# Kernel optimization log

Hardware: AMD Instinct MI355X
Metric: run time of the kernel (lower is better)

## Reference

```python
import jax, jax.numpy as jnp
import numpy as np

B, S, D = 4, 2048, 512
H, DK, DV = 8, 64, 64

def setup_inputs() -> dict:
    key = jax.random.key(0)
    ks = jax.random.split(key, 11)
    s = 0.02
    return {
        "q_in": jax.random.normal(ks[0], (B, S, D), jnp.float32),
        "k_in": jax.random.normal(ks[1], (B, S, D), jnp.float32),
        "v_in": jax.random.normal(ks[2], (B, S, D), jnp.float32),
        "Wq": jax.random.normal(ks[3], (H, D, DK), jnp.float32) * s,
        "bq": jax.random.normal(ks[4], (H, DK), jnp.float32) * s,
        "Wk": jax.random.normal(ks[5], (H, D, DK), jnp.float32) * s,
        "bk": jax.random.normal(ks[6], (H, DK), jnp.float32) * s,
        "Wv": jax.random.normal(ks[7], (H, D, DV), jnp.float32) * s,
        "bv": jax.random.normal(ks[8], (H, DV), jnp.float32) * s,
        "Wo": jax.random.normal(ks[9], (H * DV, D), jnp.float32) * s,
        "bo": jax.random.normal(ks[10], (D,), jnp.float32) * s,
    }


def reference(q_in, k_in, v_in, Wq, bq, Wk, bk, Wv, bv, Wo, bo):
    # Per-head Q/K/V projections, batched over heads (same math as the
    # original Python loop over SingleAttention heads).
    q = jnp.einsum("bsd,hdk->bhsk", q_in, Wq) + bq[None, :, None, :]   # [B,H,S,DK]
    k = jnp.einsum("bsd,hdk->bhsk", k_in, Wk) + bk[None, :, None, :]   # [B,H,S,DK]
    v = jnp.einsum("bsd,hdv->bhsv", v_in, Wv) + bv[None, :, None, :]   # [B,H,S,DV]
    scale = 1.0 / jnp.sqrt(jnp.float32(DK))
    scores = jnp.einsum("bhqk,bhsk->bhqs", q, k) * scale               # [B,H,S,S]
    attn = jax.nn.softmax(scores, axis=-1)
    out = jnp.einsum("bhqs,bhsv->bhqv", attn, v)                        # [B,H,S,DV]
    # concat heads along feature dim: [B,S,H*DV]
    concat = out.transpose(0, 2, 1, 3).reshape(B, S, H * DV)
    return concat @ Wo + bo                                             # [B,S,D]
```

## Files before the change

kernel.cpp:

```cpp
#include <hip/hip_runtime.h>
#include <hip/hip_bf16.h>

using bf16 = __hip_bfloat16;
typedef short short8  __attribute__((ext_vector_type(8)));
typedef short short4v __attribute__((ext_vector_type(4)));
typedef float float4v __attribute__((ext_vector_type(4)));

#define MFMA_BF16 __builtin_amdgcn_mfma_f32_16x16x32_bf16

#define B_  4
#define S_  2048
#define D_  512
#define H_  8
#define DK_ 64


__device__ __forceinline__ short f2bf(float f) {
  bf16 h = __float2bfloat16(f);
  return *reinterpret_cast<short*>(&h);
}

__global__ __launch_bounds__(256)
void transpose_w(const float* __restrict__ Wq, const float* __restrict__ Wk,
                 const float* __restrict__ Wv, const float* __restrict__ Wo,
                 short* __restrict__ WqT, short* __restrict__ WkT,
                 short* __restrict__ WvT, short* __restrict__ WoT) {
  __shared__ float tile[64 * 65];
  const int mat = blockIdx.y, t = blockIdx.x, tid = threadIdx.x;
  const float* W = (mat == 0) ? Wq : (mat == 1) ? Wk : (mat == 2) ? Wv : Wo;
  short* T       = (mat == 0) ? WqT : (mat == 1) ? WkT : (mat == 2) ? WvT : WoT;

  size_t sbase, ss, dbase;
  if (mat < 3) {
    int hh = t >> 3, d0 = (t & 7) * 64;
    sbase = (size_t)hh * 32768 + (size_t)d0 * 64;
    ss = 64;
    dbase = (size_t)hh * 64 * 512 + d0;
  } else {
    int n0 = (t >> 3) * 64, k0 = (t & 7) * 64;
    sbase = (size_t)k0 * 512 + n0;
    ss = 512;
    dbase = (size_t)n0 * 512 + k0;
  }

  {
    int r = tid >> 2, c0 = (tid & 3) * 16;
#pragma unroll
    for (int j = 0; j < 4; j++)
      *(float4v*)&tile[r * 65 + c0 + j * 4] =
          *(const float4v*)&W[sbase + (size_t)r * ss + c0 + j * 4];
  }
  __syncthreads();
  {
    int c = tid >> 2, r0 = (tid & 3) * 16;
#pragma unroll
    for (int j = 0; j < 2; j++) {
      short8 s;
#pragma unroll
      for (int u = 0; u < 8; u++) s[u] = f2bf(tile[(r0 + j * 8 + u) * 65 + c]);
      *(short8*)&T[dbase + (size_t)c * 512 + r0 + j * 8] = s;
    }
  }
}

__device__ __forceinline__ void gemm_core(const void* __restrict__ A,
                                          const short* __restrict__ Bt,
                                          int m0, int n0, int fp32,
                                          short* As, short* Bs,
                                          float4v acc[4][4]) {
  const int tid  = threadIdx.x;
  const int lane = tid & 63, wave = tid >> 6;
  const int quad = lane >> 4, l16 = lane & 15;
  const int wm = (wave >> 1) * 64, wn = (wave & 1) * 64;

  for (int k0 = 0; k0 < 512; k0 += 64) {
    __syncthreads();
    if (fp32) {
      const float* Af = (const float*)A;
#pragma unroll
      for (int i = 0; i < 4; i++) {
        int cid = tid + 256 * i;
        int row = cid >> 3, kc = (cid & 7) * 8;
        size_t base = (size_t)(m0 + row) * 512 + k0 + kc;
        float4v f0 = *(const float4v*)&Af[base];
        float4v f1 = *(const float4v*)&Af[base + 4];
        short8 s;
#pragma unroll
        for (int j = 0; j < 4; j++) { s[j] = f2bf(f0[j]); s[j + 4] = f2bf(f1[j]); }
        *(short8*)&As[row * 72 + kc] = s;
        *(short8*)&Bs[row * 72 + kc] =
            *(const short8*)&Bt[(size_t)(n0 + row) * 512 + k0 + kc];
      }
    } else {
      const short* Ab = (const short*)A;
#pragma unroll
      for (int i = 0; i < 4; i++) {
        int cid = tid + 256 * i;
        int row = cid >> 3, kc = (cid & 7) * 8;
        *(short8*)&As[row * 72 + kc] =
            *(const short8*)&Ab[(size_t)(m0 + row) * 512 + k0 + kc];
        *(short8*)&Bs[row * 72 + kc] =
            *(const short8*)&Bt[(size_t)(n0 + row) * 512 + k0 + kc];
      }
    }
    __syncthreads();
#pragma unroll
    for (int ks = 0; ks < 64; ks += 32) {
      short8 af[4], bfr[4];
#pragma unroll
      for (int mi = 0; mi < 4; mi++)
        af[mi] = *(short8*)&As[(wm + mi * 16 + l16) * 72 + ks + quad * 8];
#pragma unroll
      for (int ni = 0; ni < 4; ni++)
        bfr[ni] = *(short8*)&Bs[(wn + ni * 16 + l16) * 72 + ks + quad * 8];
#pragma unroll
      for (int mi = 0; mi < 4; mi++)
#pragma unroll
        for (int ni = 0; ni < 4; ni++)
          acc[mi][ni] = MFMA_BF16(af[mi], bfr[ni], acc[mi][ni], 0, 0, 0);
    }
  }
}

__global__ __launch_bounds__(256, 2)
void qkv_gemm(const float* __restrict__ qin, const float* __restrict__ kin,
              const float* __restrict__ vin,
              const short* __restrict__ WqT, const short* __restrict__ WkT,
              const short* __restrict__ WvT,
              const float* __restrict__ bq, const float* __restrict__ bk,
              const float* __restrict__ bv,
              short* __restrict__ Qp, short* __restrict__ Kp,
              short* __restrict__ Vt) {
  __shared__ __align__(16) short As[128 * 72];
  __shared__ __align__(16) short Bs[128 * 72];
  const int m0 = blockIdx.x * 128, n0 = blockIdx.y * 128;
  const int z = blockIdx.z;
  const float* A    = (z == 0) ? qin : (z == 1) ? kin : vin;
  const short* Bt   = (z == 0) ? WqT : (z == 1) ? WkT : WvT;
  const float* bias = (z == 0) ? bq  : (z == 1) ? bk  : bv;
  const float scale = (z == 0) ? 0.125f * 1.44269504088896f : 1.0f;

  float4v acc[4][4];
#pragma unroll
  for (int mi = 0; mi < 4; mi++)
#pragma unroll
    for (int ni = 0; ni < 4; ni++) acc[mi][ni] = (float4v){0.f, 0.f, 0.f, 0.f};

  gemm_core((const void*)A, Bt, m0, n0, 1, As, Bs, acc);

  const int lane = threadIdx.x & 63, wave = threadIdx.x >> 6;
  const int quad = lane >> 4, l16 = lane & 15;
  const int wm = (wave >> 1) * 64, wn = (wave & 1) * 64;

  if (z < 2) {
    short* out = (z == 0) ? Qp : Kp;
#pragma unroll
    for (int mi = 0; mi < 4; mi++) {
      int m = m0 + wm + mi * 16 + quad * 4;
      int b = m >> 11, s = m & 2047;
#pragma unroll
      for (int ni = 0; ni < 4; ni++) {
        int n = n0 + wn + ni * 16 + l16;
        int h = n >> 6, dk = n & 63;
        float bb = bias[n];
        size_t base = (((size_t)b * H_ + h) * S_ + s) * 64 + dk;
#pragma unroll
        for (int r = 0; r < 4; r++)
          out[base + (size_t)r * 64] = f2bf((acc[mi][ni][r] + bb) * scale);
      }
    }
  } else {
#pragma unroll
    for (int mi = 0; mi < 4; mi++) {
      int m = m0 + wm + mi * 16 + quad * 4;
      int b = m >> 11, s = m & 2047;
#pragma unroll
      for (int ni = 0; ni < 4; ni++) {
        int n = n0 + wn + ni * 16 + l16;
        int h = n >> 6, v = n & 63;
        float bb = bias[n];
        short4v pk;
#pragma unroll
        for (int r = 0; r < 4; r++) pk[r] = f2bf(acc[mi][ni][r] + bb);
        *(short4v*)&Vt[(((size_t)b * H_ + h) * 64 + v) * S_ + s] = pk;
      }
    }
  }
}

__global__ __launch_bounds__(256, 4)
void attn_kernel(const short* __restrict__ Qp, const short* __restrict__ Kp,
                 const short* __restrict__ Vt, short* __restrict__ Ao) {
  __shared__ __align__(16) short Ps[64 * 72];
  __shared__ __align__(16) short Ks[64 * 72];
  __shared__ __align__(16) short Vs[64 * 72];

  const int qt = blockIdx.x, bh = blockIdx.y;
  const int b = bh >> 3, h = bh & 7;
  const int tid = threadIdx.x;
  const int lane = tid & 63, wave = tid >> 6;
  const int quad = lane >> 4, l16 = lane & 15;

  const short* Qb = Qp + (size_t)bh * S_ * 64 + (size_t)qt * 64 * 64;
  const short* Kb = Kp + (size_t)bh * S_ * 64;
  const short* Vb = Vt + (size_t)bh * 64 * S_;

#pragma unroll
  for (int i = 0; i < 2; i++) {
    int cid = tid + 256 * i;
    int row = cid >> 3, kc = (cid & 7) * 8;
    *(short8*)&Ps[row * 72 + kc] = *(const short8*)&Qb[(size_t)row * 64 + kc];
  }
  __syncthreads();

  short8 qf[2];
#pragma unroll
  for (int kk = 0; kk < 2; kk++)
    qf[kk] = *(short8*)&Ps[(wave * 16 + l16) * 72 + kk * 32 + quad * 8];

  float4v lrow = (float4v){0.f, 0.f, 0.f, 0.f};
  float4v acco[4];
#pragma unroll
  for (int ni = 0; ni < 4; ni++) acco[ni] = (float4v){0.f, 0.f, 0.f, 0.f};

  short* Pw = Ps + wave * 16 * 72;

  for (int kv0 = 0; kv0 < S_; kv0 += 64) {
    __syncthreads();
#pragma unroll
    for (int i = 0; i < 2; i++) {
      int cid = tid + 256 * i;
      int row = cid >> 3, kc = (cid & 7) * 8;
      *(short8*)&Ks[row * 72 + kc] =
          *(const short8*)&Kb[(size_t)(kv0 + row) * 64 + kc];
      *(short8*)&Vs[row * 72 + kc] =
          *(const short8*)&Vb[(size_t)row * S_ + kv0 + kc];
    }
    __syncthreads();

    float4v sa[4];
#pragma unroll
    for (int ni = 0; ni < 4; ni++) sa[ni] = (float4v){0.f, 0.f, 0.f, 0.f};
#pragma unroll
    for (int kk = 0; kk < 2; kk++) {
      short8 kf[4];
#pragma unroll
      for (int ni = 0; ni < 4; ni++)
        kf[ni] = *(short8*)&Ks[(ni * 16 + l16) * 72 + kk * 32 + quad * 8];
#pragma unroll
      for (int ni = 0; ni < 4; ni++)
        sa[ni] = MFMA_BF16(qf[kk], kf[ni], sa[ni], 0, 0, 0);
    }

#pragma unroll
    for (int ni = 0; ni < 4; ni++)
#pragma unroll
      for (int r = 0; r < 4; r++) {
        float p = exp2f(sa[ni][r]);
        lrow[r] += p;
        Pw[(quad * 4 + r) * 72 + ni * 16 + l16] = f2bf(p);
      }

#pragma unroll
    for (int kks = 0; kks < 2; kks++) {
      short8 pa = *(short8*)&Pw[l16 * 72 + kks * 32 + quad * 8];
      short8 vb2[4];
#pragma unroll
      for (int ni = 0; ni < 4; ni++)
        vb2[ni] = *(short8*)&Vs[(ni * 16 + l16) * 72 + kks * 32 + quad * 8];
#pragma unroll
      for (int ni = 0; ni < 4; ni++)
        acco[ni] = MFMA_BF16(pa, vb2[ni], acco[ni], 0, 0, 0);
    }
  }

#pragma unroll
  for (int off = 1; off < 16; off <<= 1)
#pragma unroll
    for (int r = 0; r < 4; r++) lrow[r] += __shfl_xor(lrow[r], off, 16);

  const size_t obase = ((size_t)b * S_ + qt * 64 + wave * 16) * D_ + h * 64;
#pragma unroll
  for (int r = 0; r < 4; r++) {
    float li = 1.0f / lrow[r];
    int srow = quad * 4 + r;
#pragma unroll
    for (int ni = 0; ni < 4; ni++)
      Ao[obase + (size_t)srow * D_ + ni * 16 + l16] = f2bf(acco[ni][r] * li);
  }
}

__global__ __launch_bounds__(256, 2)
void out_gemm(const short* __restrict__ A, const short* __restrict__ Bt,
              const float* __restrict__ bias, float* __restrict__ out) {
  __shared__ __align__(16) short As[128 * 72];
  __shared__ __align__(16) short Bs[128 * 72];
  const int m0 = blockIdx.x * 128, n0 = blockIdx.y * 128;

  float4v acc[4][4];
#pragma unroll
  for (int mi = 0; mi < 4; mi++)
#pragma unroll
    for (int ni = 0; ni < 4; ni++) acc[mi][ni] = (float4v){0.f, 0.f, 0.f, 0.f};

  gemm_core((const void*)A, Bt, m0, n0, 0, As, Bs, acc);

  const int lane = threadIdx.x & 63, wave = threadIdx.x >> 6;
  const int quad = lane >> 4, l16 = lane & 15;
  const int wm = (wave >> 1) * 64, wn = (wave & 1) * 64;
#pragma unroll
  for (int mi = 0; mi < 4; mi++) {
    int m = m0 + wm + mi * 16 + quad * 4;
#pragma unroll
    for (int ni = 0; ni < 4; ni++) {
      int n = n0 + wn + ni * 16 + l16;
      float bb = bias[n];
#pragma unroll
      for (int r = 0; r < 4; r++)
        out[(size_t)(m + r) * 512 + n] = acc[mi][ni][r] + bb;
    }
  }
}

extern "C" void kernel_launch(void* const* d_in, const int* in_sizes, int n_in,
                              void* d_out, int out_size, void* d_ws, size_t ws_size,
                              hipStream_t stream) {
  const float* qin = (const float*)d_in[0];
  const float* kin = (const float*)d_in[1];
  const float* vin = (const float*)d_in[2];
  const float* Wq  = (const float*)d_in[3];
  const float* bq  = (const float*)d_in[4];
  const float* Wk  = (const float*)d_in[5];
  const float* bk  = (const float*)d_in[6];
  const float* Wv  = (const float*)d_in[7];
  const float* bv  = (const float*)d_in[8];
  const float* Wo  = (const float*)d_in[9];
  const float* bo  = (const float*)d_in[10];
  float* out = (float*)d_out;
  short* ws  = (short*)d_ws;

  const size_t NTOK = (size_t)B_ * S_ * D_;
  short* Qp  = ws;
  short* Kp  = ws + NTOK;
  short* Vt  = ws + 2 * NTOK;
  short* Ao  = ws + 3 * NTOK;
  short* WqT = ws + 4 * NTOK;
  short* WkT = WqT + 512 * 512;
  short* WvT = WkT + 512 * 512;
  short* WoT = WvT + 512 * 512;

  transpose_w<<<dim3(64, 4), 256, 0, stream>>>(Wq, Wk, Wv, Wo,
                                               WqT, WkT, WvT, WoT);
  qkv_gemm<<<dim3(64, 4, 3), 256, 0, stream>>>(qin, kin, vin, WqT, WkT, WvT,
                                               bq, bk, bv, Qp, Kp, Vt);
  attn_kernel<<<dim3(32, 32), 256, 0, stream>>>(Qp, Kp, Vt, Ao);
  out_gemm<<<dim3(64, 4), 256, 0, stream>>>(Ao, WoT, bo, out);
}
```

Baseline: 220.6 us.

## Rewrite attention kernel with 32x32 MFMA, async double-buffered LDS, register-resident P

The attention kernel now uses 32x32x16 MFMAs with 128 query rows per block (32 per wave). K/V tiles are double-buffered through direct global-to-LDS loads into XOR-swizzled shared memory. Q fragments are loaded straight from global into registers, and P is repacked with cvt_pk and permlane32_swap instead of a round trip through LDS. The change also remaps blocks so neighbouring blocks share a head, and adds s_setprio hints. These aim to cut LDS traffic, barriers and load latency, at the cost of higher register pressure and fewer blocks in the grid.

```diff
diff --git a/kernel.cpp b/kernel.cpp
--- a/kernel.cpp
+++ b/kernel.cpp
@@ -5,8 +5,11 @@
 typedef short short8  __attribute__((ext_vector_type(8)));
 typedef short short4v __attribute__((ext_vector_type(4)));
 typedef float float4v __attribute__((ext_vector_type(4)));
-
-#define MFMA_BF16 __builtin_amdgcn_mfma_f32_16x16x32_bf16
+typedef float f32x16  __attribute__((ext_vector_type(16)));
+typedef unsigned int uint4v __attribute__((ext_vector_type(4)));
+
+#define MFMA_BF16   __builtin_amdgcn_mfma_f32_16x16x32_bf16
+#define MFMA32_BF16 __builtin_amdgcn_mfma_f32_32x32x16_bf16
 
 #define B_  4
 #define S_  2048
@@ -18,6 +21,23 @@
 __device__ __forceinline__ short f2bf(float f) {
   bf16 h = __float2bfloat16(f);
   return *reinterpret_cast<short*>(&h);
+}
+
+__device__ __forceinline__ unsigned cvtpk(float lo, float hi) {
+  unsigned r;
+  asm("v_cvt_pk_bf16_f32 %0, %1, %2" : "=v"(r) : "v"(lo), "v"(hi));
+  return r;
+}
+
+__device__ __forceinline__ void plswap(unsigned& a, unsigned& b) {
+  asm("v_permlane32_swap_b32 %0, %1" : "+v"(a), "+v"(b));
+}
+
+__device__ __forceinline__ short8 mk8(unsigned v0, unsigned v1, unsigned v2,
+                                      unsigned v3) {
+  uint4v u;
+  u[0] = v0; u[1] = v1; u[2] = v2; u[3] = v3;
+  return __builtin_bit_cast(short8, u);
 }
 
 __global__ __launch_bounds__(256)
@@ -191,102 +211,129 @@
 __global__ __launch_bounds__(256, 4)
 void attn_kernel(const short* __restrict__ Qp, const short* __restrict__ Kp,
                  const short* __restrict__ Vt, short* __restrict__ Ao) {
-  __shared__ __align__(16) short Ps[64 * 72];
-  __shared__ __align__(16) short Ks[64 * 72];
-  __shared__ __align__(16) short Vs[64 * 72];
-
-  const int qt = blockIdx.x, bh = blockIdx.y;
+  __shared__ __align__(16) short Ksh[2][4096];
+  __shared__ __align__(16) short Vsh[2][4096];
+
+  const int orig = blockIdx.y * gridDim.x + blockIdx.x;
+  const int lb = (orig & 7) * 64 + (orig >> 3);
+  const int qt = lb & 15, bh = lb >> 4;
   const int b = bh >> 3, h = bh & 7;
+
   const int tid = threadIdx.x;
   const int lane = tid & 63, wave = tid >> 6;
-  const int quad = lane >> 4, l16 = lane & 15;
-
-  const short* Qb = Qp + (size_t)bh * S_ * 64 + (size_t)qt * 64 * 64;
+  const int l31 = lane & 31, hi = lane >> 5, s7 = l31 & 7;
+
+  const short* Qb = Qp + (size_t)bh * S_ * 64;
   const short* Kb = Kp + (size_t)bh * S_ * 64;
   const short* Vb = Vt + (size_t)bh * 64 * S_;
 
-#pragma unroll
-  for (int i = 0; i < 2; i++) {
-    int cid = tid + 256 * i;
-    int row = cid >> 3, kc = (cid & 7) * 8;
-    *(short8*)&Ps[row * 72 + kc] = *(const short8*)&Qb[(size_t)row * 64 + kc];
+  short8 qf[4];
+  {
+    const short* qrow = Qb + (size_t)(qt * 128 + wave * 32 + l31) * 64;
+#pragma unroll
+    for (int w = 0; w < 4; w++)
+      qf[w] = *(const short8*)&qrow[w * 16 + hi * 8];
+  }
+
+  const int slot0 = wave * 128 + lane;
+  const int kr0 = slot0 >> 3, kc0 = slot0 & 7;
+  const int kr1 = kr0 + 8;
+  const short* kg0 = Kb + (size_t)kr0 * 64 + ((kc0 ^ (kr0 & 7)) << 3);
+  const short* kg1 = Kb + (size_t)kr1 * 64 + ((kc0 ^ (kr1 & 7)) << 3);
+  const short* vg0 = Vb + (size_t)kr0 * S_ + ((kc0 ^ (kr0 & 7)) << 3);
+  const short* vg1 = Vb + (size_t)kr1 * S_ + ((kc0 ^ (kr1 & 7)) << 3);
+
+#define GLL(g, l) __builtin_amdgcn_global_load_lds(                        \
+      (const __attribute__((address_space(1))) void*)(g),                  \
+      (__attribute__((address_space(3))) void*)(l), 16, 0, 0)
+
+  f32x16 acc0, acc1;
+#pragma unroll
+  for (int r = 0; r < 16; r++) { acc0[r] = 0.f; acc1[r] = 0.f; }
+  float ls0 = 0.f, ls1 = 0.f;
+
+  {
+    short* kd = &Ksh[0][wave * 1024];
+    short* vd = &Vsh[0][wave * 1024];
+    GLL(kg0, kd); GLL(kg1, kd + 512);
+    GLL(vg0, vd); GLL(vg1, vd + 512);
   }
   __syncthreads();
 
-  short8 qf[2];
-#pragma unroll
-  for (int kk = 0; kk < 2; kk++)
-    qf[kk] = *(short8*)&Ps[(wave * 16 + l16) * 72 + kk * 32 + quad * 8];
-
-  float4v lrow = (float4v){0.f, 0.f, 0.f, 0.f};
-  float4v acco[4];
-#pragma unroll
-  for (int ni = 0; ni < 4; ni++) acco[ni] = (float4v){0.f, 0.f, 0.f, 0.f};
-
-  short* Pw = Ps + wave * 16 * 72;
-
-  for (int kv0 = 0; kv0 < S_; kv0 += 64) {
+  for (int t = 0; t < 32; t++) {
+    const int cur = t & 1;
+    if (t < 31) {
+      short* kd = &Ksh[cur ^ 1][wave * 1024];
+      short* vd = &Vsh[cur ^ 1][wave * 1024];
+      GLL(kg0 + (size_t)(t + 1) * 4096, kd);
+      GLL(kg1 + (size_t)(t + 1) * 4096, kd + 512);
+      GLL(vg0 + (size_t)(t + 1) * 64, vd);
+      GLL(vg1 + (size_t)(t + 1) * 64, vd + 512);
+    }
+    const short* kb = Ksh[cur];
+    const short* vs = Vsh[cur];
+
+#pragma unroll
+    for (int kt = 0; kt < 2; kt++) {
+      f32x16 sa;
+#pragma unroll
+      for (int r = 0; r < 16; r++) sa[r] = 0.f;
+      __builtin_amdgcn_s_setprio(1);
+#pragma unroll
+      for (int w = 0; w < 4; w++) {
+        short8 kf = *(const short8*)&kb[(kt * 32 + l31) * 64 +
+                                        (((2 * w + hi) ^ s7) << 3)];
+        sa = MFMA32_BF16(kf, qf[w], sa, 0, 0, 0);
+      }
+      __builtin_amdgcn_s_setprio(0);
+
+      float pv[16];
+#pragma unroll
+      for (int r = 0; r < 16; r++) pv[r] = exp2f(sa[r]);
+#pragma unroll
+      for (int r = 0; r < 8; r++) { ls0 += pv[r]; ls1 += pv[r + 8]; }
+
+      unsigned a0 = cvtpk(pv[0], pv[1]),  b0 = cvtpk(pv[4], pv[5]);
+      plswap(a0, b0);
+      unsigned c0 = cvtpk(pv[2], pv[3]),  d0 = cvtpk(pv[6], pv[7]);
+      plswap(c0, d0);
+      short8 pa0 = mk8(a0, c0, b0, d0);
+      unsigned a1 = cvtpk(pv[8], pv[9]),  b1 = cvtpk(pv[12], pv[13]);
+      plswap(a1, b1);
+      unsigned c1 = cvtpk(pv[10], pv[11]), d1 = cvtpk(pv[14], pv[15]);
+      plswap(c1, d1);
+      short8 pa1 = mk8(a1, c1, b1, d1);
+
+      __builtin_amdgcn_s_setprio(1);
+      {
+        const int kw0 = kt * 2, kw1 = kt * 2 + 1;
+        short8 v00 = *(const short8*)&vs[l31 * 64 + (((2 * kw0 + hi) ^ s7) << 3)];
+        short8 v10 = *(const short8*)&vs[(32 + l31) * 64 + (((2 * kw0 + hi) ^ s7) << 3)];
+        acc0 = MFMA32_BF16(pa0, v00, acc0, 0, 0, 0);
+        acc1 = MFMA32_BF16(pa0, v10, acc1, 0, 0, 0);
+        short8 v01 = *(const short8*)&vs[l31 * 64 + (((2 * kw1 + hi) ^ s7) << 3)];
+        short8 v11 = *(const short8*)&vs[(32 + l31) * 64 + (((2 * kw1 + hi) ^ s7) << 3)];
+        acc0 = MFMA32_BF16(pa1, v01, acc0, 0, 0, 0);
+        acc1 = MFMA32_BF16(pa1, v11, acc1, 0, 0, 0);
+      }
+      __builtin_amdgcn_s_setprio(0);
+    }
     __syncthreads();
-#pragma unroll
-    for (int i = 0; i < 2; i++) {
-      int cid = tid + 256 * i;
-      int row = cid >> 3, kc = (cid & 7) * 8;
-      *(short8*)&Ks[row * 72 + kc] =
-          *(const short8*)&Kb[(size_t)(kv0 + row) * 64 + kc];
-      *(short8*)&Vs[row * 72 + kc] =
-          *(const short8*)&Vb[(size_t)row * S_ + kv0 + kc];
-    }
-    __syncthreads();
-
-    float4v sa[4];
-#pragma unroll
-    for (int ni = 0; ni < 4; ni++) sa[ni] = (float4v){0.f, 0.f, 0.f, 0.f};
-#pragma unroll
-    for (int kk = 0; kk < 2; kk++) {
-      short8 kf[4];
-#pragma unroll
-      for (int ni = 0; ni < 4; ni++)
-        kf[ni] = *(short8*)&Ks[(ni * 16 + l16) * 72 + kk * 32 + quad * 8];
-#pragma unroll
-      for (int ni = 0; ni < 4; ni++)
-        sa[ni] = MFMA_BF16(qf[kk], kf[ni], sa[ni], 0, 0, 0);
-    }
-
-#pragma unroll
-    for (int ni = 0; ni < 4; ni++)
-#pragma unroll
-      for (int r = 0; r < 4; r++) {
-        float p = exp2f(sa[ni][r]);
-        lrow[r] += p;
-        Pw[(quad * 4 + r) * 72 + ni * 16 + l16] = f2bf(p);
-      }
-
-#pragma unroll
-    for (int kks = 0; kks < 2; kks++) {
-      short8 pa = *(short8*)&Pw[l16 * 72 + kks * 32 + quad * 8];
-      short8 vb2[4];
-#pragma unroll
-      for (int ni = 0; ni < 4; ni++)
-        vb2[ni] = *(short8*)&Vs[(ni * 16 + l16) * 72 + kks * 32 + quad * 8];
-#pragma unroll
-      for (int ni = 0; ni < 4; ni++)
-        acco[ni] = MFMA_BF16(pa, vb2[ni], acco[ni], 0, 0, 0);
-    }
-  }
-
-#pragma unroll
-  for (int off = 1; off < 16; off <<= 1)
-#pragma unroll
-    for (int r = 0; r < 4; r++) lrow[r] += __shfl_xor(lrow[r], off, 16);
-
-  const size_t obase = ((size_t)b * S_ + qt * 64 + wave * 16) * D_ + h * 64;
-#pragma unroll
-  for (int r = 0; r < 4; r++) {
-    float li = 1.0f / lrow[r];
-    int srow = quad * 4 + r;
-#pragma unroll
-    for (int ni = 0; ni < 4; ni++)
-      Ao[obase + (size_t)srow * D_ + ni * 16 + l16] = f2bf(acco[ni][r] * li);
+  }
+#undef GLL
+
+  float lsum = ls0 + ls1;
+  lsum += __shfl_xor(lsum, 32, 64);
+  float myrl = 1.0f / lsum;
+
+  const size_t obase =
+      ((size_t)b * S_ + (size_t)(qt * 128 + wave * 32)) * D_ + h * 64 + l31;
+#pragma unroll
+  for (int r = 0; r < 16; r++) {
+    int q = (r & 3) + 8 * (r >> 2) + 4 * hi;
+    float rl = __shfl(myrl, q, 64);
+    Ao[obase + (size_t)q * D_]      = f2bf(acc0[r] * rl);
+    Ao[obase + (size_t)q * D_ + 32] = f2bf(acc1[r] * rl);
   }
 }
 
@@ -353,6 +400,6 @@
                                                WqT, WkT, WvT, WoT);
   qkv_gemm<<<dim3(64, 4, 3), 256, 0, stream>>>(qin, kin, vin, WqT, WkT, WvT,
                                                bq, bk, bv, Qp, Kp, Vt);
-  attn_kernel<<<dim3(32, 32), 256, 0, stream>>>(Qp, Kp, Vt, Ao);
+  attn_kernel<<<dim3(16, 32), 256, 0, stream>>>(Qp, Kp, Vt, Ao);
   out_gemm<<<dim3(64, 4), 256, 0, stream>>>(Ao, WoT, bo, out);
 }
```

Measured after the change: 208.3 us. 1.06x faster.
